# Kernel optimization log

Hardware: AMD Instinct MI355X
Metric: run time of the kernel (lower is better)

Reference implementation:

```python
import jax, jax.numpy as jnp
import numpy as np

T, B, D, H = 512, 256, 256, 64  # time, batch, input_dim, hidden_dim == n_qubits


def setup_inputs() -> dict:
    key = jax.random.key(0)
    ks = jax.random.split(key, 5)
    inputs = jax.random.normal(ks[0], (T, B, D), dtype=jnp.float32)
    # 4 gate linear layers: Linear(D+H -> H), stacked [4, D+H, H]
    s1 = 1.0 / np.sqrt(D + H)
    W_gates = jax.random.uniform(ks[1], (4, D + H, H), minval=-s1, maxval=s1, dtype=jnp.float32)
    b_gates = jax.random.uniform(ks[2], (4, H), minval=-s1, maxval=s1, dtype=jnp.float32)
    # QLayer surrogate per gate: linear H -> H (variational circuit stand-in)
    s2 = 1.0 / np.sqrt(H)
    Wq = jax.random.uniform(ks[3], (4, H, H), minval=-s2, maxval=s2, dtype=jnp.float32)
    bq = jax.random.uniform(ks[4], (4, H), minval=-s2, maxval=s2, dtype=jnp.float32)
    return {"inputs": inputs, "W_gates": W_gates, "b_gates": b_gates, "Wq": Wq, "bq": bq}


def reference(inputs, W_gates, b_gates, Wq, bq):
    Bsz = inputs.shape[1]
    h0 = jnp.zeros((Bsz, H), dtype=inputs.dtype)
    c0 = jnp.zeros((Bsz, H), dtype=inputs.dtype)

    def step(carry, x_t):
        hx, cx = carry
        comb = jnp.concatenate([x_t, hx], axis=1)          # [B, D+H]
        z = jnp.einsum('bd,gdh->gbh', comb, W_gates) + b_gates[:, None, :]  # 4 gate linears
        q = jnp.einsum('gbh,ghk->gbk', z, Wq) + bq[:, None, :]              # QLayer per gate
        f = jax.nn.sigmoid(q[0])
        i = jax.nn.sigmoid(q[1])
        g = jnp.tanh(q[2])
        o = jax.nn.sigmoid(q[3])
        cx = f * cx + i * g
        hx = o * jnp.tanh(cx)
        return (hx, cx), hx

    (hx, cx), outputs = jax.lax.scan(step, (h0, c0), inputs)
    return outputs, hx, cx
```

## Files before the change

### kernel.cpp

```cpp
#include <hip/hip_runtime.h>
#include <hip/hip_bf16.h>

#define T_STEPS 512
#define BATCH 256
#define DIN 256
#define HID 64
#define NCOL 256
#define CHUNK_MAX 512

typedef __attribute__((ext_vector_type(8))) short short8;
typedef __attribute__((ext_vector_type(4))) float f32x4;

__device__ __forceinline__ ushort bfr(float f) {
    __hip_bfloat16 h = __float2bfloat16(f);
    ushort u; __builtin_memcpy(&u, &h, 2); return u;
}
__device__ __forceinline__ float bff(ushort u) {
    unsigned v = (unsigned)u << 16; float f; __builtin_memcpy(&f, &v, 4); return f;
}


__global__ __launch_bounds__(256) void precompute_kernel(
    const float* __restrict__ Wg, const float* __restrict__ bg,
    const float* __restrict__ Wq, const float* __restrict__ bq,
    ushort* __restrict__ WbfT, float* __restrict__ Whq, float* __restrict__ beff)
{
    int idx = blockIdx.x * 256 + threadIdx.x;
    if (idx < 65536) {
        int n = idx >> 8, k = idx & 255, g = n >> 6, h = n & 63;
        const float* wg = Wg + (size_t)g * 320 * 64 + (size_t)k * 64;
        const float* wq = Wq + (size_t)g * 4096 + h;
        float s = 0.f;
        #pragma unroll 8
        for (int j = 0; j < 64; ++j) s += wg[j] * wq[(size_t)j * 64];
        WbfT[idx] = bfr(s);
    } else if (idx < 65536 + 16384) {
        int r = idx - 65536;
        int k = r >> 8, col = r & 255, g = col >> 6, h = col & 63;
        const float* wg = Wg + (size_t)g * 320 * 64 + (size_t)(256 + k) * 64;
        const float* wq = Wq + (size_t)g * 4096 + h;
        float s = 0.f;
        #pragma unroll 8
        for (int j = 0; j < 64; ++j) s += wg[j] * wq[(size_t)j * 64];
        Whq[r] = s;
    } else if (idx < 65536 + 16384 + 256) {
        int col = idx - 65536 - 16384;
        int g = col >> 6, h = col & 63;
        const float* wq = Wq + (size_t)g * 4096 + h;
        const float* bgp = bg + g * 64;
        float s = bq[g * 64 + h];
        for (int j = 0; j < 64; ++j) s += bgp[j] * wq[(size_t)j * 64];
        beff[col] = s;
    }
}

__global__ __launch_bounds__(256) void xproj_mfma(
    const float* __restrict__ A, const ushort* __restrict__ BT,
    const float* __restrict__ beff, float* __restrict__ C)
{
    __shared__ ushort Ah[128 * 64];
    __shared__ ushort Al[128 * 64];
    __shared__ ushort Bs[256 * 64];
    const int tid = threadIdx.x;
    const int wave = tid >> 6, lane = tid & 63;
    const int mb = blockIdx.x;
    const float* Ab = A + (size_t)mb * 128 * 256;

    f32x4 acc[2][16];
    #pragma unroll
    for (int m = 0; m < 2; ++m)
        #pragma unroll
        for (int n = 0; n < 16; ++n) acc[m][n] = (f32x4){0.f, 0.f, 0.f, 0.f};

    for (int k0 = 0; k0 < 256; k0 += 64) {
        #pragma unroll
        for (int it = 0; it < 4; ++it) {
            int li = tid + it * 256;
            int row = li >> 3, c2 = li & 7;
            const float4 f0 = *reinterpret_cast<const float4*>(Ab + (size_t)row * 256 + k0 + c2 * 8);
            const float4 f1 = *reinterpret_cast<const float4*>(Ab + (size_t)row * 256 + k0 + c2 * 8 + 4);
            float fs[8] = {f0.x, f0.y, f0.z, f0.w, f1.x, f1.y, f1.z, f1.w};
            short8 hi, lo;
            #pragma unroll
            for (int j = 0; j < 8; ++j) {
                ushort h = bfr(fs[j]);
                hi[j] = (short)h;
                lo[j] = (short)bfr(fs[j] - bff(h));
            }
            int dst = (row * 128 + c2 * 16) ^ ((row & 7) << 4);
            *reinterpret_cast<short8*>((char*)Ah + dst) = hi;
            *reinterpret_cast<short8*>((char*)Al + dst) = lo;
        }
        #pragma unroll
        for (int it = 0; it < 8; ++it) {
            int li = tid + it * 256;
            int row = li >> 3, c = li & 7;
            short8 v = *reinterpret_cast<const short8*>(BT + (size_t)row * 256 + k0 + c * 8);
            int dst = (row * 128 + c * 16) ^ ((row & 7) << 4);
            *reinterpret_cast<short8*>((char*)Bs + dst) = v;
        }
        __syncthreads();
        #pragma unroll
        for (int ks = 0; ks < 2; ++ks) {
            const int kk = ks * 32 + (lane >> 4) * 8;
            short8 a_h[2], a_l[2];
            #pragma unroll
            for (int mf = 0; mf < 2; ++mf) {
                int row = wave * 32 + mf * 16 + (lane & 15);
                int off = (row * 128 + kk * 2) ^ ((row & 7) << 4);
                a_h[mf] = *reinterpret_cast<const short8*>((char*)Ah + off);
                a_l[mf] = *reinterpret_cast<const short8*>((char*)Al + off);
            }
            #pragma unroll
            for (int nf = 0; nf < 16; ++nf) {
                int col = nf * 16 + (lane & 15);
                int boff = (col * 128 + kk * 2) ^ ((col & 7) << 4);
                short8 b = *reinterpret_cast<const short8*>((char*)Bs + boff);
                #pragma unroll
                for (int mf = 0; mf < 2; ++mf) {
                    acc[mf][nf] = __builtin_amdgcn_mfma_f32_16x16x32_bf16(a_h[mf], b, acc[mf][nf], 0, 0, 0);
                    acc[mf][nf] = __builtin_amdgcn_mfma_f32_16x16x32_bf16(a_l[mf], b, acc[mf][nf], 0, 0, 0);
                }
            }
        }
        __syncthreads();
    }
    #pragma unroll
    for (int nf = 0; nf < 16; ++nf) {
        int col = nf * 16 + (lane & 15);
        float bias = beff[col];
        #pragma unroll
        for (int mf = 0; mf < 2; ++mf) {
            int r0 = mb * 128 + wave * 32 + mf * 16 + (lane >> 4) * 4;
            #pragma unroll
            for (int j = 0; j < 4; ++j)
                C[(size_t)(r0 + j) * 256 + col] = acc[mf][nf][j] + bias;
        }
    }
}

__global__ __launch_bounds__(256) void lstm_seq(
    const float* __restrict__ Xq, const float* __restrict__ Whq,
    float* __restrict__ out, float* __restrict__ hx, float* __restrict__ cx,
    int nsteps, int t0, int first)
{
    __shared__ float act_s[2][256];
    const int b = blockIdx.x;
    const int tid = threadIdx.x;
    const int lane = tid & 63, wave = tid >> 6;

    float wcol[64];
    #pragma unroll
    for (int k = 0; k < 64; ++k) wcol[k] = Whq[k * 256 + tid];

    float c_reg, hn;
    if (first) { c_reg = 0.f; hn = 0.f; }
    else { c_reg = cx[b * 64 + lane]; hn = hx[b * 64 + lane]; }

    const float* xrow = Xq + (size_t)b * 256 + tid;
    float xq0 = xrow[0];
    float xq1 = (nsteps > 1) ? xrow[(size_t)BATCH * NCOL] : 0.f;

    for (int tl = 0; tl < nsteps; ++tl) {
        float xq2 = (tl + 2 < nsteps) ? xrow[(size_t)(tl + 2) * BATCH * NCOL] : 0.f;
        const int p = tl & 1;
        unsigned hu = __float_as_uint(hn);
        float a0 = 0.f, a1 = 0.f, a2 = 0.f, a3 = 0.f;
        #pragma unroll
        for (int k = 0; k < 64; k += 4) {
            a0 += __uint_as_float(__builtin_amdgcn_readlane(hu, k + 0)) * wcol[k + 0];
            a1 += __uint_as_float(__builtin_amdgcn_readlane(hu, k + 1)) * wcol[k + 1];
            a2 += __uint_as_float(__builtin_amdgcn_readlane(hu, k + 2)) * wcol[k + 2];
            a3 += __uint_as_float(__builtin_amdgcn_readlane(hu, k + 3)) * wcol[k + 3];
        }
        float q = xq0 + ((a0 + a1) + (a2 + a3));
        float act;
        if (wave == 2) act = 1.f - 2.f / (__expf(q + q) + 1.f);
        else           act = 1.f / (1.f + __expf(-q));
        act_s[p][tid] = act;
        asm volatile("s_waitcnt lgkmcnt(0)\n\ts_barrier" ::: "memory");
        float f  = act_s[p][lane];
        float ii = act_s[p][64 + lane];
        float gg = act_s[p][128 + lane];
        float oo = act_s[p][192 + lane];
        c_reg = f * c_reg + ii * gg;
        hn = oo * (1.f - 2.f / (__expf(c_reg + c_reg) + 1.f));
        if (wave == 0) out[((size_t)(t0 + tl) * BATCH + b) * HID + lane] = hn;
        xq0 = xq1; xq1 = xq2;
    }
    if (wave == 0) {
        cx[b * 64 + lane] = c_reg;
        hx[b * 64 + lane] = hn;
    }
}

extern "C" void kernel_launch(void* const* d_in, const int* in_sizes, int n_in,
                              void* d_out, int out_size, void* d_ws, size_t ws_size,
                              hipStream_t stream) {
    const float* inputs = (const float*)d_in[0];
    const float* Wg = (const float*)d_in[1];
    const float* bg = (const float*)d_in[2];
    const float* Wq = (const float*)d_in[3];
    const float* bq = (const float*)d_in[4];

    float* out = (float*)d_out;
    float* hx = out + (size_t)T_STEPS * BATCH * HID;
    float* cx = hx + BATCH * HID;

    char* ws = (char*)d_ws;
    ushort* WbfT = (ushort*)ws;
    float* Whq  = (float*)(ws + 131072);
    float* beff = (float*)(ws + 196608);
    float* Xq   = (float*)(ws + 197632);

    const size_t head_bytes = 197632;
    const size_t per_step = (size_t)BATCH * NCOL * 4;
    int Tc = 1;
    if (ws_size > head_bytes) {
        size_t fit = (ws_size - head_bytes) / per_step;
        if (fit < 1) fit = 1;
        if (fit > CHUNK_MAX) fit = CHUNK_MAX;
        Tc = (int)fit;
    }

    precompute_kernel<<<dim3(321), dim3(256), 0, stream>>>(Wg, bg, Wq, bq, WbfT, Whq, beff);

    int first = 1;
    for (int t0 = 0; t0 < T_STEPS; t0 += Tc) {
        int cur = (T_STEPS - t0 < Tc) ? (T_STEPS - t0) : Tc;
        xproj_mfma<<<dim3(cur * 2), dim3(256), 0, stream>>>(
            inputs + (size_t)t0 * BATCH * DIN, WbfT, beff, Xq);
        lstm_seq<<<dim3(256), dim3(256), 0, stream>>>(
            Xq, Whq, out, hx, cx, cur, t0, first);
        first = 0;
    }
}
```

Baseline: 635.4 us.

## Remap gate columns per wave and exchange gates via shuffles instead of LDS

Each wave now holds all four gates for 16 hidden units, so the gate combine runs within a wave using shuffles rather than through LDS. Only the new hidden state is written to LDS, and the next step reads it back as float4 broadcasts instead of 64 readlanes. The sigmoid and tanh paths are merged into one branch-free form using a per-lane scale. Each step still needs one barrier, and the 16 lanes per group doing the cell update are duplicated work.

```diff
diff --git a/kernel.cpp b/kernel.cpp
--- a/kernel.cpp
+++ b/kernel.cpp
@@ -144,53 +144,66 @@
     float* __restrict__ out, float* __restrict__ hx, float* __restrict__ cx,
     int nsteps, int t0, int first)
 {
-    __shared__ float act_s[2][256];
+    __shared__ float h_lds[2][64];
     const int b = blockIdx.x;
     const int tid = threadIdx.x;
-    const int lane = tid & 63, wave = tid >> 6;
+    const int l = tid & 63, w = tid >> 6;
+    const int l15 = l & 15, g = l >> 4;
+    const int hidx = w * 16 + l15;
+    const int col = g * 64 + hidx;
 
     float wcol[64];
     #pragma unroll
-    for (int k = 0; k < 64; ++k) wcol[k] = Whq[k * 256 + tid];
-
-    float c_reg, hn;
-    if (first) { c_reg = 0.f; hn = 0.f; }
-    else { c_reg = cx[b * 64 + lane]; hn = hx[b * 64 + lane]; }
-
-    const float* xrow = Xq + (size_t)b * 256 + tid;
-    float xq0 = xrow[0];
-    float xq1 = (nsteps > 1) ? xrow[(size_t)BATCH * NCOL] : 0.f;
+    for (int k = 0; k < 64; ++k) wcol[k] = Whq[k * 256 + col];
+
+    const float gs = (g == 2) ? 2.0f : 1.0f;
+    const float gofs = gs - 1.0f;
+
+    float c_reg, hn = 0.f;
+    if (first) {
+        c_reg = 0.f;
+        if (g == 0) h_lds[0][hidx] = 0.f;
+    } else {
+        c_reg = cx[b * 64 + hidx];
+        if (g == 0) h_lds[0][hidx] = hx[b * 64 + hidx];
+    }
+    __syncthreads();
+
+    const float* xcol = Xq + (size_t)b * NCOL + col;
+    float xq0 = xcol[0];
+    float xq1 = (nsteps > 1) ? xcol[(size_t)BATCH * NCOL] : 0.f;
 
     for (int tl = 0; tl < nsteps; ++tl) {
-        float xq2 = (tl + 2 < nsteps) ? xrow[(size_t)(tl + 2) * BATCH * NCOL] : 0.f;
+        float xq2 = (tl + 2 < nsteps) ? xcol[(size_t)(tl + 2) * BATCH * NCOL] : 0.f;
         const int p = tl & 1;
-        unsigned hu = __float_as_uint(hn);
         float a0 = 0.f, a1 = 0.f, a2 = 0.f, a3 = 0.f;
         #pragma unroll
-        for (int k = 0; k < 64; k += 4) {
-            a0 += __uint_as_float(__builtin_amdgcn_readlane(hu, k + 0)) * wcol[k + 0];
-            a1 += __uint_as_float(__builtin_amdgcn_readlane(hu, k + 1)) * wcol[k + 1];
-            a2 += __uint_as_float(__builtin_amdgcn_readlane(hu, k + 2)) * wcol[k + 2];
-            a3 += __uint_as_float(__builtin_amdgcn_readlane(hu, k + 3)) * wcol[k + 3];
+        for (int k4 = 0; k4 < 16; ++k4) {
+            float4 hv = *reinterpret_cast<const float4*>(&h_lds[p][k4 << 2]);
+            a0 += hv.x * wcol[4 * k4 + 0];
+            a1 += hv.y * wcol[4 * k4 + 1];
+            a2 += hv.z * wcol[4 * k4 + 2];
+            a3 += hv.w * wcol[4 * k4 + 3];
         }
         float q = xq0 + ((a0 + a1) + (a2 + a3));
-        float act;
-        if (wave == 2) act = 1.f - 2.f / (__expf(q + q) + 1.f);
-        else           act = 1.f / (1.f + __expf(-q));
-        act_s[p][tid] = act;
+        float s = 1.f / (1.f + __expf(-q * gs));
+        float act = s * gs - gofs;
+        float fA = __shfl(act, l15 +  0, 64);
+        float iA = __shfl(act, l15 + 16, 64);
+        float gA = __shfl(act, l15 + 32, 64);
+        float oA = __shfl(act, l15 + 48, 64);
+        c_reg = fA * c_reg + iA * gA;
+        hn = oA * (1.f - 2.f / (__expf(c_reg + c_reg) + 1.f));
+        if (g == 0) {
+            h_lds[p ^ 1][hidx] = hn;
+            out[((size_t)(t0 + tl) * BATCH + b) * HID + hidx] = hn;
+        }
         asm volatile("s_waitcnt lgkmcnt(0)\n\ts_barrier" ::: "memory");
-        float f  = act_s[p][lane];
-        float ii = act_s[p][64 + lane];
-        float gg = act_s[p][128 + lane];
-        float oo = act_s[p][192 + lane];
-        c_reg = f * c_reg + ii * gg;
-        hn = oo * (1.f - 2.f / (__expf(c_reg + c_reg) + 1.f));
-        if (wave == 0) out[((size_t)(t0 + tl) * BATCH + b) * HID + lane] = hn;
         xq0 = xq1; xq1 = xq2;
     }
-    if (wave == 0) {
-        cx[b * 64 + lane] = c_reg;
-        hx[b * 64 + lane] = hn;
+    if (g == 0) {
+        cx[b * 64 + hidx] = c_reg;
+        hx[b * 64 + hidx] = hn;
     }
 }
 
```

After: 524.6 us. 17.4% less time.
